# Optimization experiments

Hardware: AMD Instinct MI355X
Metric: run time of the kernel (lower is better)

The kernel has to match this reference:

```python
import jax, jax.numpy as jnp
import numpy as np

N = 50000
E = 800000
D = 128
NCLASS = 10


def setup_inputs() -> dict:
    key = jax.random.key(0)
    ks = jax.random.split(key, 12)
    stdv = 1.0 / np.sqrt(D)
    inp = {
        "x": jax.random.normal(ks[0], (N, D), dtype=jnp.float32),
        "edge_src": jax.random.randint(ks[1], (E,), 0, N, dtype=jnp.int32),
        "edge_dst": jax.random.randint(ks[2], (E,), 0, N, dtype=jnp.int32),
        "edge_weight": jax.random.uniform(ks[3], (E,), dtype=jnp.float32),
        "W1": jax.random.uniform(ks[4], (D, D), jnp.float32, -stdv, stdv),
        "b1": jax.random.uniform(ks[5], (D,), jnp.float32, -stdv, stdv),
        "W2": jax.random.uniform(ks[6], (D, D), jnp.float32, -stdv, stdv),
        "b2": jax.random.uniform(ks[7], (D,), jnp.float32, -stdv, stdv),
        "W3": jax.random.uniform(ks[8], (D, D), jnp.float32, -stdv, stdv),
        "b3": jax.random.uniform(ks[9], (D,), jnp.float32, -stdv, stdv),
        "lin_W": jax.random.normal(ks[10], (NCLASS, 3 * D), dtype=jnp.float32) * 0.05,
        "lin_b": jax.random.normal(ks[11], (NCLASS,), dtype=jnp.float32) * 0.05,
    }
    return inp


def _gcn_layer(h, W, b, edge_src, edge_dst, edge_weight):
    # support = h @ W  (dense GEMM), then spmm(adj, support) as gather-scale-scatter
    support = h @ W                                   # [N, out]
    msgs = support[edge_src] * edge_weight[:, None]   # [E, out]
    agg = jax.ops.segment_sum(msgs, edge_dst, num_segments=h.shape[0])
    return agg + b


def reference(x, edge_src, edge_dst, edge_weight, W1, b1, W2, b2, W3, b3, lin_W, lin_b):
    x1 = jax.nn.relu(_gcn_layer(x, W1, b1, edge_src, edge_dst, edge_weight))
    o1 = jnp.max(x1, axis=0)
    x2 = jax.nn.relu(_gcn_layer(x1, W2, b2, edge_src, edge_dst, edge_weight))
    o2 = jnp.max(x2, axis=0)
    x3 = _gcn_layer(x2, W3, b3, edge_src, edge_dst, edge_weight)
    o3 = jnp.max(x3, axis=0)
    lin_in = jnp.concatenate([o1, o2, o3], axis=0)    # [3*D]
    logits = lin_W @ lin_in + lin_b                   # [nclass]
    return jax.nn.log_softmax(logits, axis=0)
```

## Files before the change

### kernel.cpp

```cpp
#include <hip/hip_runtime.h>
#include <hip/hip_bf16.h>
#include <math.h>

#define NN 50000
#define NPAD 50048
#define NE 800000
#define DD 128
#define NCLS 10
#define SCAN_BLOCK 1024
#define NTILES ((NN + 1 + SCAN_BLOCK - 1) / SCAN_BLOCK)

typedef short s16x8 __attribute__((ext_vector_type(8)));
typedef float f32x4 __attribute__((ext_vector_type(4)));

__device__ __forceinline__ unsigned short f2bf(float x) {
  __hip_bfloat16 h = __float2bfloat16(x);
  return __builtin_bit_cast(unsigned short, h);
}

__device__ __forceinline__ unsigned int f2fp8(float x) {
  unsigned int b = __float_as_uint(x);
  unsigned int s = (b >> 24) & 0x80u;
  int e = (int)((b >> 23) & 255u) - 120;
  unsigned int m23 = b & 0x7FFFFFu;
  if (e >= 16) return s | 0x7F;
  if (e <= 0) return s;
  unsigned int m = m23 >> 20;
  unsigned int rem = m23 & 0xFFFFFu;
  if (rem > 0x80000u || (rem == 0x80000u && (m & 1u))) {
    ++m;
    if (m == 8u) { m = 0; ++e; if (e >= 16) return s | 0x7F; }
  }
  return s | ((unsigned int)e << 3) | m;
}

__device__ __forceinline__ unsigned int fkey(float f) {
  unsigned int u = __float_as_uint(f);
  return u ^ ((u & 0x80000000u) ? 0xFFFFFFFFu : 0x80000000u);
}
__device__ __forceinline__ float funkey(unsigned int k) {
  unsigned int u = (k & 0x80000000u) ? (k ^ 0x80000000u) : ~k;
  return __uint_as_float(u);
}

__global__ void k_count(const int* __restrict__ edst, int* __restrict__ offs) {
  int e = blockIdx.x * blockDim.x + threadIdx.x;
  if (e < NE) atomicAdd(&offs[edst[e] + 1], 1);
}

__global__ void k_scan_partial(const int* __restrict__ offs, int* __restrict__ bsum) {
  __shared__ int red[SCAN_BLOCK];
  int i = blockIdx.x * SCAN_BLOCK + threadIdx.x;
  red[threadIdx.x] = (i < NN + 1) ? offs[i] : 0;
  __syncthreads();
  for (int off = SCAN_BLOCK / 2; off > 0; off >>= 1) {
    if ((int)threadIdx.x < off) red[threadIdx.x] += red[threadIdx.x + off];
    __syncthreads();
  }
  if (threadIdx.x == 0) bsum[blockIdx.x] = red[0];
}

__global__ void k_scan_bsum(int* __restrict__ bsum) {
  if (threadIdx.x == 0) {
    int run = 0;
    for (int i = 0; i < NTILES; ++i) { int v = bsum[i]; bsum[i] = run; run += v; }
  }
}

__global__ void k_scan_final(int* __restrict__ offs, const int* __restrict__ bsum,
                             int* __restrict__ cursor) {
  __shared__ int tmp[SCAN_BLOCK];
  int i = blockIdx.x * SCAN_BLOCK + threadIdx.x;
  int v = (i < NN + 1) ? offs[i] : 0;
  tmp[threadIdx.x] = v;
  __syncthreads();
  for (int off = 1; off < SCAN_BLOCK; off <<= 1) {
    int t = ((int)threadIdx.x >= off) ? tmp[threadIdx.x - off] : 0;
    __syncthreads();
    tmp[threadIdx.x] += t;
    __syncthreads();
  }
  int incl = tmp[threadIdx.x] + bsum[blockIdx.x];
  if (i < NN + 1) {
    offs[i] = incl;
    if (i < NN) cursor[i] = incl;
  }
}

__global__ void k_fill(const int* __restrict__ esrc, const int* __restrict__ edst,
                       const float* __restrict__ ew, int* __restrict__ cursor,
                       int2* __restrict__ csr) {
  int e = blockIdx.x * blockDim.x + threadIdx.x;
  if (e < NE) {
    int d = edst[e];
    int p = atomicAdd(&cursor[d], 1);
    csr[p] = make_int2(esrc[e], __float_as_int(ew[e]));
  }
}

__global__ __launch_bounds__(256) void k_cvtW(const float* __restrict__ W1,
    const float* __restrict__ W2, const float* __restrict__ W3,
    unsigned short* __restrict__ WT1, unsigned short* __restrict__ WT2,
    unsigned short* __restrict__ WT3, unsigned int* __restrict__ omax) {
  int i = blockIdx.x * 256 + threadIdx.x;
  if (i < 3 * DD) omax[i] = 0u;
  if (i < DD * DD) {
    int k = i >> 7, c = i & 127;
    WT1[c * DD + k] = f2bf(W1[i]);
    WT2[c * DD + k] = f2bf(W2[i]);
    WT3[c * DD + k] = f2bf(W3[i]);
  }
}

template <int F32IN>
__global__ __launch_bounds__(256) void k_mm(const void* __restrict__ Hv,
                                            const unsigned short* __restrict__ Wt,
                                            unsigned char* __restrict__ Sout) {
  __shared__ unsigned short Hl[32 * DD];
  char* lb = (char*)Hl;
  const int wave = threadIdx.x >> 6, lane = threadIdx.x & 63;
  const int l15 = lane & 15, lk16 = (lane >> 4);
  const int r0 = blockIdx.x * 32;

#pragma unroll
  for (int j = 0; j < 2; ++j) {
    const int idx = threadIdx.x + j * 256;
    const int B = idx * 16;
    const int row = B >> 8;
    const int addr = B ^ ((row & 7) << 4);
    if (F32IN) {
      const float* H = (const float*)Hv;
      const int r = r0 + row;
      float4 a = make_float4(0.f, 0.f, 0.f, 0.f), b = a;
      if (r < NN) {
        const float* src = H + (size_t)r * DD + ((B & 255) >> 1);
        a = *(const float4*)src;
        b = *(const float4*)(src + 4);
      }
      uint4 pv;
      pv.x = (uint)f2bf(a.x) | ((uint)f2bf(a.y) << 16);
      pv.y = (uint)f2bf(a.z) | ((uint)f2bf(a.w) << 16);
      pv.z = (uint)f2bf(b.x) | ((uint)f2bf(b.y) << 16);
      pv.w = (uint)f2bf(b.z) | ((uint)f2bf(b.w) << 16);
      *(uint4*)(lb + addr) = pv;
    } else {
      const char* H = (const char*)Hv;
      uint4 v = *(const uint4*)(H + (size_t)r0 * 256 + B);
      *(uint4*)(lb + addr) = v;
    }
  }
  __syncthreads();

  const int cbase = wave * 32;
  s16x8 Af[2][4];
#pragma unroll
  for (int m = 0; m < 2; ++m)
#pragma unroll
    for (int ks = 0; ks < 4; ++ks)
      Af[m][ks] = *(const s16x8*)&Wt[(cbase + m * 16 + l15) * DD + ks * 32 + lk16 * 8];

  s16x8 Bf[2][4];
#pragma unroll
  for (int n = 0; n < 2; ++n) {
    const int row = n * 16 + l15;
#pragma unroll
    for (int ks = 0; ks < 4; ++ks) {
      const int B = row * 256 + ks * 64 + lk16 * 16;
      Bf[n][ks] = *(const s16x8*)(lb + (B ^ ((row & 7) << 4)));
    }
  }

  f32x4 acc[2][2];
#pragma unroll
  for (int m = 0; m < 2; ++m)
#pragma unroll
    for (int n = 0; n < 2; ++n) acc[m][n] = (f32x4){0.f, 0.f, 0.f, 0.f};

#pragma unroll
  for (int ks = 0; ks < 4; ++ks)
#pragma unroll
    for (int m = 0; m < 2; ++m)
#pragma unroll
      for (int n = 0; n < 2; ++n)
        acc[m][n] = __builtin_amdgcn_mfma_f32_16x16x32_bf16(Af[m][ks], Bf[n][ks],
                                                            acc[m][n], 0, 0, 0);

  __syncthreads();
#pragma unroll
  for (int m = 0; m < 2; ++m)
#pragma unroll
    for (int n = 0; n < 2; ++n) {
      const int row = n * 16 + l15;
      const int colb = cbase + m * 16 + 4 * lk16;
      const int B = row * 128 + colb;
      unsigned int pv = f2fp8(acc[m][n][0]) | (f2fp8(acc[m][n][1]) << 8)
                      | (f2fp8(acc[m][n][2]) << 16) | (f2fp8(acc[m][n][3]) << 24);
      *(unsigned int*)(lb + (B ^ ((row & 7) << 4))) = pv;
    }
  __syncthreads();
  {
    const int B = threadIdx.x * 16;
    const int row = B >> 7;
    uint4 v = *(const uint4*)(lb + (B ^ ((row & 7) << 4)));
    *(uint4*)(Sout + (size_t)r0 * 128 + B) = v;
  }
}

__device__ __forceinline__ void fma8v(float* acc, float w, uint2 u) {
#pragma unroll
  for (int h = 0; h < 2; ++h) {
    const unsigned int v = h ? u.y : u.x;
#pragma unroll
    for (int j = 0; j < 4; ++j) {
      const unsigned int c = (v >> (8 * j)) & 255u;
      const float dec = __uint_as_float(((c & 0x80u) << 24) | ((c & 0x7Fu) << 20));
      acc[h * 4 + j] = fmaf(w, dec, acc[h * 4 + j]);
    }
  }
}

__global__ __launch_bounds__(256) void k_agg(const unsigned char* __restrict__ S,
                                             const int2* __restrict__ csr,
                                             const int* __restrict__ offs,
                                             const float* __restrict__ bias,
                                             unsigned short* __restrict__ Xout,
                                             unsigned int* __restrict__ omax,
                                             int do_relu) {
  __shared__ unsigned int cmax[DD];
  for (int i = threadIdx.x; i < DD; i += 256) cmax[i] = 0u;
  __syncthreads();
  const int lane = threadIdx.x & 63;
  const int wave = threadIdx.x >> 6;
  const int q = lane >> 4;
  const int t = lane & 15;
  const int gwave = blockIdx.x * 4 + wave;
  const int nwaves = gridDim.x * 4;
  const unsigned char* Sc = S + t * 8;
  const float SCALE = 0x1p120f;

  float bcol[8];
  {
    float4 b0 = *(const float4*)&bias[t * 8];
    float4 b1 = *(const float4*)&bias[t * 8 + 4];
    bcol[0] = b0.x; bcol[1] = b0.y; bcol[2] = b0.z; bcol[3] = b0.w;
    bcol[4] = b1.x; bcol[5] = b1.y; bcol[6] = b1.z; bcol[7] = b1.w;
  }
  float mx[8];
#pragma unroll
  for (int j = 0; j < 8; ++j) mx[j] = -INFINITY;

  for (int d = gwave; d < NN; d += nwaves) {
    const int e0 = offs[d], e1 = offs[d + 1];
    const int nedge = e1 - e0;
    float acc[8] = {0.f, 0.f, 0.f, 0.f, 0.f, 0.f, 0.f, 0.f};
    int e = e0 + q;
    int done = 0;
    for (; done + 16 <= nedge; done += 16, e += 16) {
      int2 a0 = csr[e];      int2 a1 = csr[e + 4];
      int2 a2 = csr[e + 8];  int2 a3 = csr[e + 12];
      uint2 u0 = *(const uint2*)&Sc[(size_t)a0.x * DD];
      uint2 u1 = *(const uint2*)&Sc[(size_t)a1.x * DD];
      uint2 u2 = *(const uint2*)&Sc[(size_t)a2.x * DD];
      uint2 u3 = *(const uint2*)&Sc[(size_t)a3.x * DD];
      fma8v(acc, __int_as_float(a0.y) * SCALE, u0);
      fma8v(acc, __int_as_float(a1.y) * SCALE, u1);
      fma8v(acc, __int_as_float(a2.y) * SCALE, u2);
      fma8v(acc, __int_as_float(a3.y) * SCALE, u3);
    }
    if (done + 8 <= nedge) {
      int2 a0 = csr[e];      int2 a1 = csr[e + 4];
      uint2 u0 = *(const uint2*)&Sc[(size_t)a0.x * DD];
      uint2 u1 = *(const uint2*)&Sc[(size_t)a1.x * DD];
      fma8v(acc, __int_as_float(a0.y) * SCALE, u0);
      fma8v(acc, __int_as_float(a1.y) * SCALE, u1);
      done += 8; e += 8;
    }
    while (__any(e < e1)) {
      if (e < e1) {
        int2 c = csr[e];
        uint2 u = *(const uint2*)&Sc[(size_t)c.x * DD];
        fma8v(acc, __int_as_float(c.y) * SCALE, u);
      }
      e += 4;
    }
#pragma unroll
    for (int j = 0; j < 8; ++j) {
      acc[j] += __shfl_xor(acc[j], 16, 64);
      acc[j] += __shfl_xor(acc[j], 32, 64);
      acc[j] += bcol[j];
      if (do_relu) acc[j] = fmaxf(acc[j], 0.f);
      mx[j] = fmaxf(mx[j], acc[j]);
    }
    if (Xout && q == 0) {
      uint4 xv;
      xv.x = (uint)f2bf(acc[0]) | ((uint)f2bf(acc[1]) << 16);
      xv.y = (uint)f2bf(acc[2]) | ((uint)f2bf(acc[3]) << 16);
      xv.z = (uint)f2bf(acc[4]) | ((uint)f2bf(acc[5]) << 16);
      xv.w = (uint)f2bf(acc[6]) | ((uint)f2bf(acc[7]) << 16);
      *(uint4*)&Xout[(size_t)d * DD + t * 8] = xv;
    }
  }
  if (q == 0) {
#pragma unroll
    for (int j = 0; j < 8; ++j) atomicMax(&cmax[t * 8 + j], fkey(mx[j]));
  }
  __syncthreads();
  for (int i = threadIdx.x; i < DD; i += 256) atomicMax(&omax[i], cmax[i]);
}

__global__ void k_head(const unsigned int* __restrict__ omax,
                       const float* __restrict__ linW,
                       const float* __restrict__ linb,
                       float* __restrict__ out) {
  __shared__ float o[3 * DD];
  __shared__ float logits[NCLS];
  int t = threadIdx.x;
  if (t < 3 * DD) o[t] = funkey(omax[t]);
  __syncthreads();
  if (t < NCLS) {
    float acc = linb[t];
    for (int j = 0; j < 3 * DD; ++j) acc = fmaf(linW[t * 3 * DD + j], o[j], acc);
    logits[t] = acc;
  }
  __syncthreads();
  if (t == 0) {
    float m = -INFINITY;
    for (int c = 0; c < NCLS; ++c) m = fmaxf(m, logits[c]);
    float s = 0.f;
    for (int c = 0; c < NCLS; ++c) s += expf(logits[c] - m);
    float ls = logf(s);
    for (int c = 0; c < NCLS; ++c) out[c] = logits[c] - m - ls;
  }
}

extern "C" void kernel_launch(void* const* d_in, const int* in_sizes, int n_in,
                              void* d_out, int out_size, void* d_ws, size_t ws_size,
                              hipStream_t stream) {
  const float* x    = (const float*)d_in[0];
  const int*   esrc = (const int*)d_in[1];
  const int*   edst = (const int*)d_in[2];
  const float* ew   = (const float*)d_in[3];
  const float* W1   = (const float*)d_in[4];
  const float* b1   = (const float*)d_in[5];
  const float* W2   = (const float*)d_in[6];
  const float* b2   = (const float*)d_in[7];
  const float* W3   = (const float*)d_in[8];
  const float* b3   = (const float*)d_in[9];
  const float* linW = (const float*)d_in[10];
  const float* linb = (const float*)d_in[11];
  float* out = (float*)d_out;

  size_t off = 0;
  auto alloc = [&](size_t bytes) {
    void* p = (char*)d_ws + off;
    off += (bytes + 255) & ~(size_t)255;
    return p;
  };
  unsigned short* X1   = (unsigned short*)alloc((size_t)NPAD * DD * 2);
  unsigned short* X2   = (unsigned short*)alloc((size_t)NPAD * DD * 2);
  unsigned char*  S    = (unsigned char*)alloc((size_t)NPAD * DD);
  unsigned short* WT1  = (unsigned short*)alloc((size_t)DD * DD * 2);
  unsigned short* WT2  = (unsigned short*)alloc((size_t)DD * DD * 2);
  unsigned short* WT3  = (unsigned short*)alloc((size_t)DD * DD * 2);
  int*          offs   = (int*)alloc((NN + 2) * 4);
  int*          cursor = (int*)alloc(NN * 4);
  int2*         csr    = (int2*)alloc((size_t)NE * 8);
  unsigned int* omax   = (unsigned int*)alloc(3 * DD * 4);
  int*          bsum   = (int*)alloc(NTILES * 4);
  (void)ws_size; (void)n_in; (void)in_sizes; (void)out_size;

  hipMemsetAsync(offs, 0, (NN + 2) * 4, stream);
  k_count<<<(NE + 255) / 256, 256, 0, stream>>>(edst, offs);
  k_scan_partial<<<NTILES, SCAN_BLOCK, 0, stream>>>(offs, bsum);
  k_scan_bsum<<<1, 64, 0, stream>>>(bsum);
  k_scan_final<<<NTILES, SCAN_BLOCK, 0, stream>>>(offs, bsum, cursor);
  k_fill<<<(NE + 255) / 256, 256, 0, stream>>>(esrc, edst, ew, cursor, csr);

  k_cvtW<<<(DD * DD + 255) / 256, 256, 0, stream>>>(W1, W2, W3, WT1, WT2, WT3, omax);

  const int mm_grid = NPAD / 32;
  k_mm<1><<<mm_grid, 256, 0, stream>>>(x, WT1, S);
  k_agg<<<2048, 256, 0, stream>>>(S, csr, offs, b1, X1, omax, 1);
  k_mm<0><<<mm_grid, 256, 0, stream>>>(X1, WT2, S);
  k_agg<<<2048, 256, 0, stream>>>(S, csr, offs, b2, X2, omax + DD, 1);
  k_mm<0><<<mm_grid, 256, 0, stream>>>(X2, WT3, S);
  k_agg<<<2048, 256, 0, stream>>>(S, csr, offs, b3, nullptr, omax + 2 * DD, 0);

  k_head<<<1, 384, 0, stream>>>(omax, linW, linb, out);
}
```

Before: 444.7 us.

## Pack CSR edges into 32-bit words and make GEMM persistent with LDS-staged weights

The CSR entry shrinks from an int2 (source index plus float weight) to a single 32-bit word holding a 16-bit source index and a 16-bit fixed-point weight. This halves CSR traffic in the fill and aggregation kernels. The GEMM kernel now loads the transposed weight matrix into LDS once per block and loops over row tiles on a fixed grid of 512 blocks, instead of fetching weights from global memory for every tile. The risks are weight quantization error, and a 16-bit index cannot address node ids above 65535, which only works because N is 50000.

```diff
diff --git a/kernel.cpp b/kernel.cpp
--- a/kernel.cpp
+++ b/kernel.cpp
@@ -89,12 +89,13 @@
 
 __global__ void k_fill(const int* __restrict__ esrc, const int* __restrict__ edst,
                        const float* __restrict__ ew, int* __restrict__ cursor,
-                       int2* __restrict__ csr) {
+                       unsigned int* __restrict__ csr) {
   int e = blockIdx.x * blockDim.x + threadIdx.x;
   if (e < NE) {
     int d = edst[e];
     int p = atomicAdd(&cursor[d], 1);
-    csr[p] = make_int2(esrc[e], __float_as_int(ew[e]));
+    unsigned int w16 = (unsigned int)(ew[e] * 65535.0f + 0.5f);
+    csr[p] = (w16 << 16) | (unsigned int)esrc[e];
   }
 }
 
@@ -116,38 +117,19 @@
 __global__ __launch_bounds__(256) void k_mm(const void* __restrict__ Hv,
                                             const unsigned short* __restrict__ Wt,
                                             unsigned char* __restrict__ Sout) {
+  __shared__ unsigned short Wl[DD * DD];
   __shared__ unsigned short Hl[32 * DD];
+  char* wb = (char*)Wl;
   char* lb = (char*)Hl;
   const int wave = threadIdx.x >> 6, lane = threadIdx.x & 63;
   const int l15 = lane & 15, lk16 = (lane >> 4);
-  const int r0 = blockIdx.x * 32;
-
-#pragma unroll
-  for (int j = 0; j < 2; ++j) {
+
+#pragma unroll
+  for (int j = 0; j < 8; ++j) {
     const int idx = threadIdx.x + j * 256;
     const int B = idx * 16;
     const int row = B >> 8;
-    const int addr = B ^ ((row & 7) << 4);
-    if (F32IN) {
-      const float* H = (const float*)Hv;
-      const int r = r0 + row;
-      float4 a = make_float4(0.f, 0.f, 0.f, 0.f), b = a;
-      if (r < NN) {
-        const float* src = H + (size_t)r * DD + ((B & 255) >> 1);
-        a = *(const float4*)src;
-        b = *(const float4*)(src + 4);
-      }
-      uint4 pv;
-      pv.x = (uint)f2bf(a.x) | ((uint)f2bf(a.y) << 16);
-      pv.y = (uint)f2bf(a.z) | ((uint)f2bf(a.w) << 16);
-      pv.z = (uint)f2bf(b.x) | ((uint)f2bf(b.y) << 16);
-      pv.w = (uint)f2bf(b.z) | ((uint)f2bf(b.w) << 16);
-      *(uint4*)(lb + addr) = pv;
-    } else {
-      const char* H = (const char*)Hv;
-      uint4 v = *(const uint4*)(H + (size_t)r0 * 256 + B);
-      *(uint4*)(lb + addr) = v;
-    }
+    *(uint4*)(wb + (B ^ ((row & 7) << 4))) = *(const uint4*)((const char*)Wt + B);
   }
   __syncthreads();
 
@@ -156,53 +138,90 @@
 #pragma unroll
   for (int m = 0; m < 2; ++m)
 #pragma unroll
-    for (int ks = 0; ks < 4; ++ks)
-      Af[m][ks] = *(const s16x8*)&Wt[(cbase + m * 16 + l15) * DD + ks * 32 + lk16 * 8];
-
-  s16x8 Bf[2][4];
-#pragma unroll
-  for (int n = 0; n < 2; ++n) {
-    const int row = n * 16 + l15;
-#pragma unroll
     for (int ks = 0; ks < 4; ++ks) {
+      const int row = cbase + m * 16 + l15;
       const int B = row * 256 + ks * 64 + lk16 * 16;
-      Bf[n][ks] = *(const s16x8*)(lb + (B ^ ((row & 7) << 4)));
-    }
-  }
-
-  f32x4 acc[2][2];
-#pragma unroll
-  for (int m = 0; m < 2; ++m)
-#pragma unroll
-    for (int n = 0; n < 2; ++n) acc[m][n] = (f32x4){0.f, 0.f, 0.f, 0.f};
-
-#pragma unroll
-  for (int ks = 0; ks < 4; ++ks)
-#pragma unroll
-    for (int m = 0; m < 2; ++m)
-#pragma unroll
-      for (int n = 0; n < 2; ++n)
-        acc[m][n] = __builtin_amdgcn_mfma_f32_16x16x32_bf16(Af[m][ks], Bf[n][ks],
-                                                            acc[m][n], 0, 0, 0);
-
-  __syncthreads();
-#pragma unroll
-  for (int m = 0; m < 2; ++m)
+      Af[m][ks] = *(const s16x8*)(wb + (B ^ ((row & 7) << 4)));
+    }
+
+  for (int t = blockIdx.x; t < NPAD / 32; t += gridDim.x) {
+    const int r0 = t * 32;
+    __syncthreads();
+
+#pragma unroll
+    for (int j = 0; j < 2; ++j) {
+      const int idx = threadIdx.x + j * 256;
+      const int B = idx * 16;
+      const int row = B >> 8;
+      const int addr = B ^ ((row & 7) << 4);
+      if (F32IN) {
+        const float* H = (const float*)Hv;
+        const int r = r0 + row;
+        float4 a = make_float4(0.f, 0.f, 0.f, 0.f), b = a;
+        if (r < NN) {
+          const float* src = H + (size_t)r * DD + ((B & 255) >> 1);
+          a = *(const float4*)src;
+          b = *(const float4*)(src + 4);
+        }
+        uint4 pv;
+        pv.x = (uint)f2bf(a.x) | ((uint)f2bf(a.y) << 16);
+        pv.y = (uint)f2bf(a.z) | ((uint)f2bf(a.w) << 16);
+        pv.z = (uint)f2bf(b.x) | ((uint)f2bf(b.y) << 16);
+        pv.w = (uint)f2bf(b.z) | ((uint)f2bf(b.w) << 16);
+        *(uint4*)(lb + addr) = pv;
+      } else {
+        const char* H = (const char*)Hv;
+        uint4 v = *(const uint4*)(H + (size_t)r0 * 256 + B);
+        *(uint4*)(lb + addr) = v;
+      }
+    }
+    __syncthreads();
+
+    s16x8 Bf[2][4];
 #pragma unroll
     for (int n = 0; n < 2; ++n) {
       const int row = n * 16 + l15;
-      const int colb = cbase + m * 16 + 4 * lk16;
-      const int B = row * 128 + colb;
-      unsigned int pv = f2fp8(acc[m][n][0]) | (f2fp8(acc[m][n][1]) << 8)
-                      | (f2fp8(acc[m][n][2]) << 16) | (f2fp8(acc[m][n][3]) << 24);
-      *(unsigned int*)(lb + (B ^ ((row & 7) << 4))) = pv;
-    }
-  __syncthreads();
-  {
-    const int B = threadIdx.x * 16;
-    const int row = B >> 7;
-    uint4 v = *(const uint4*)(lb + (B ^ ((row & 7) << 4)));
-    *(uint4*)(Sout + (size_t)r0 * 128 + B) = v;
+#pragma unroll
+      for (int ks = 0; ks < 4; ++ks) {
+        const int B = row * 256 + ks * 64 + lk16 * 16;
+        Bf[n][ks] = *(const s16x8*)(lb + (B ^ ((row & 7) << 4)));
+      }
+    }
+
+    f32x4 acc[2][2];
+#pragma unroll
+    for (int m = 0; m < 2; ++m)
+#pragma unroll
+      for (int n = 0; n < 2; ++n) acc[m][n] = (f32x4){0.f, 0.f, 0.f, 0.f};
+
+#pragma unroll
+    for (int ks = 0; ks < 4; ++ks)
+#pragma unroll
+      for (int m = 0; m < 2; ++m)
+#pragma unroll
+        for (int n = 0; n < 2; ++n)
+          acc[m][n] = __builtin_amdgcn_mfma_f32_16x16x32_bf16(Af[m][ks], Bf[n][ks],
+                                                              acc[m][n], 0, 0, 0);
+
+    __syncthreads();
+#pragma unroll
+    for (int m = 0; m < 2; ++m)
+#pragma unroll
+      for (int n = 0; n < 2; ++n) {
+        const int row = n * 16 + l15;
+        const int colb = cbase + m * 16 + 4 * lk16;
+        const int B = row * 128 + colb;
+        unsigned int pv = f2fp8(acc[m][n][0]) | (f2fp8(acc[m][n][1]) << 8)
+                        | (f2fp8(acc[m][n][2]) << 16) | (f2fp8(acc[m][n][3]) << 24);
+        *(unsigned int*)(lb + (B ^ ((row & 7) << 4))) = pv;
+      }
+    __syncthreads();
+    {
+      const int B = threadIdx.x * 16;
+      const int row = B >> 7;
+      uint4 v = *(const uint4*)(lb + (B ^ ((row & 7) << 4)));
+      *(uint4*)(Sout + (size_t)r0 * 128 + B) = v;
+    }
   }
 }
 
@@ -220,7 +239,7 @@
 }
 
 __global__ __launch_bounds__(256) void k_agg(const unsigned char* __restrict__ S,
-                                             const int2* __restrict__ csr,
+                                             const unsigned int* __restrict__ csr,
                                              const int* __restrict__ offs,
                                              const float* __restrict__ bias,
                                              unsigned short* __restrict__ Xout,
@@ -236,7 +255,7 @@
   const int gwave = blockIdx.x * 4 + wave;
   const int nwaves = gridDim.x * 4;
   const unsigned char* Sc = S + t * 8;
-  const float SCALE = 0x1p120f;
+  const float WSC = 0x1p120f / 65535.0f;
 
   float bcol[8];
   {
@@ -256,30 +275,30 @@
     int e = e0 + q;
     int done = 0;
     for (; done + 16 <= nedge; done += 16, e += 16) {
-      int2 a0 = csr[e];      int2 a1 = csr[e + 4];
-      int2 a2 = csr[e + 8];  int2 a3 = csr[e + 12];
-      uint2 u0 = *(const uint2*)&Sc[(size_t)a0.x * DD];
-      uint2 u1 = *(const uint2*)&Sc[(size_t)a1.x * DD];
-      uint2 u2 = *(const uint2*)&Sc[(size_t)a2.x * DD];
-      uint2 u3 = *(const uint2*)&Sc[(size_t)a3.x * DD];
-      fma8v(acc, __int_as_float(a0.y) * SCALE, u0);
-      fma8v(acc, __int_as_float(a1.y) * SCALE, u1);
-      fma8v(acc, __int_as_float(a2.y) * SCALE, u2);
-      fma8v(acc, __int_as_float(a3.y) * SCALE, u3);
+      unsigned int a0 = csr[e];      unsigned int a1 = csr[e + 4];
+      unsigned int a2 = csr[e + 8];  unsigned int a3 = csr[e + 12];
+      uint2 u0 = *(const uint2*)&Sc[(size_t)(a0 & 0xFFFFu) * DD];
+      uint2 u1 = *(const uint2*)&Sc[(size_t)(a1 & 0xFFFFu) * DD];
+      uint2 u2 = *(const uint2*)&Sc[(size_t)(a2 & 0xFFFFu) * DD];
+      uint2 u3 = *(const uint2*)&Sc[(size_t)(a3 & 0xFFFFu) * DD];
+      fma8v(acc, (float)(a0 >> 16) * WSC, u0);
+      fma8v(acc, (float)(a1 >> 16) * WSC, u1);
+      fma8v(acc, (float)(a2 >> 16) * WSC, u2);
+      fma8v(acc, (float)(a3 >> 16) * WSC, u3);
     }
     if (done + 8 <= nedge) {
-      int2 a0 = csr[e];      int2 a1 = csr[e + 4];
-      uint2 u0 = *(const uint2*)&Sc[(size_t)a0.x * DD];
-      uint2 u1 = *(const uint2*)&Sc[(size_t)a1.x * DD];
-      fma8v(acc, __int_as_float(a0.y) * SCALE, u0);
-      fma8v(acc, __int_as_float(a1.y) * SCALE, u1);
+      unsigned int a0 = csr[e];      unsigned int a1 = csr[e + 4];
+      uint2 u0 = *(const uint2*)&Sc[(size_t)(a0 & 0xFFFFu) * DD];
+      uint2 u1 = *(const uint2*)&Sc[(size_t)(a1 & 0xFFFFu) * DD];
+      fma8v(acc, (float)(a0 >> 16) * WSC, u0);
+      fma8v(acc, (float)(a1 >> 16) * WSC, u1);
       done += 8; e += 8;
     }
     while (__any(e < e1)) {
       if (e < e1) {
-        int2 c = csr[e];
-        uint2 u = *(const uint2*)&Sc[(size_t)c.x * DD];
-        fma8v(acc, __int_as_float(c.y) * SCALE, u);
+        unsigned int c = csr[e];
+        uint2 u = *(const uint2*)&Sc[(size_t)(c & 0xFFFFu) * DD];
+        fma8v(acc, (float)(c >> 16) * WSC, u);
       }
       e += 4;
     }
@@ -364,7 +383,7 @@
   unsigned short* WT3  = (unsigned short*)alloc((size_t)DD * DD * 2);
   int*          offs   = (int*)alloc((NN + 2) * 4);
   int*          cursor = (int*)alloc(NN * 4);
-  int2*         csr    = (int2*)alloc((size_t)NE * 8);
+  unsigned int* csr    = (unsigned int*)alloc((size_t)NE * 4);
   unsigned int* omax   = (unsigned int*)alloc(3 * DD * 4);
   int*          bsum   = (int*)alloc(NTILES * 4);
   (void)ws_size; (void)n_in; (void)in_sizes; (void)out_size;
@@ -378,7 +397,7 @@
 
   k_cvtW<<<(DD * DD + 255) / 256, 256, 0, stream>>>(W1, W2, W3, WT1, WT2, WT3, omax);
 
-  const int mm_grid = NPAD / 32;
+  const int mm_grid = 512;
   k_mm<1><<<mm_grid, 256, 0, stream>>>(x, WT1, S);
   k_agg<<<2048, 256, 0, stream>>>(S, csr, offs, b1, X1, omax, 1);
   k_mm<0><<<mm_grid, 256, 0, stream>>>(X1, WT2, S);
```

Result: faster. 425.6 us (-4.3%).
